# Kernel tuning notes

Hardware: AMD Instinct MI355X
Metric: run time of the kernel (lower is better)

The kernel has to match this reference:

```python
import jax, jax.numpy as jnp
import numpy as np

NB, NL, V, VOCAB, D, TOPK = 16, 64, 16384, 32000, 256, 16
NITER, EARLY, RW = 8, 2, 0.8


def setup_inputs():
    key = jax.random.key(0)
    ks = jax.random.split(key, 8)
    probas = jax.random.uniform(ks[0], (NB, NL, V), dtype=jnp.float32) + 1e-6
    h_d = jax.random.normal(ks[1], (NB, NL, D), dtype=jnp.float32)
    lengths = jax.random.randint(ks[2], (NB,), NL // 2, NL + 1)
    mask = (jnp.arange(NL)[None, :] < lengths[:, None]).astype(jnp.int32)  # prefix mask
    batch_vocab = jax.random.randint(ks[3], (V,), 0, VOCAB)
    emb_table = jax.random.normal(ks[4], (VOCAB, D), dtype=jnp.float32) * 0.02
    W1 = jax.random.normal(ks[5], (2 * D, D), dtype=jnp.float32) * 0.006
    b1 = jnp.zeros((D,), dtype=jnp.float32)
    return {"probas": probas, "h_d": h_d, "mask": mask, "batch_vocab": batch_vocab,
            "emb_table": emb_table, "W1": W1, "b1": b1}


def _forward(probas, h_d, mask, batch_vocab, emb_table, W1, b1):
    maskf = mask.astype(probas.dtype)
    MAP = jnp.argmax(probas, axis=-1)                       # [nb,nl]
    topk_vals, topk_idx = jax.lax.top_k(probas, TOPK)       # [nb,nl,K]
    topk_vals = jnp.where(mask[..., None] < 1, 1.0, topk_vals)
    logits = jnp.log(topk_vals)                             # Categorical(probs) == categorical(log p)
    sLens = jnp.sum(mask, axis=1)                           # [nb]
    one_hot = jnp.arange(NL)[None, :] == (sLens - 1)[:, None]  # one_hot_by_mask: last valid pos
    m2d = (mask[:, :, None] * mask[:, None, :]) > 0
    eyeM = jnp.eye(NL, dtype=probas.dtype)
    h_masked = h_d * maskf[..., None]

    def step(carry, k):
        max_score, best, count, stopped = carry
        choice = jax.random.categorical(k, logits)          # [nb,nl]
        samples = jnp.take_along_axis(topk_idx, choice[..., None], axis=-1)[..., 0]
        samples = jnp.where(one_hot, MAP, samples)
        embs = emb_table[batch_vocab[samples]] * maskf[..., None]   # gather+embed, masked
        new_embs = jax.nn.relu(jnp.concatenate([embs, h_masked], axis=-1) @ W1 + b1)
        Kmat = jnp.einsum('bld,bmd->blm', new_embs, new_embs)       # [nb,nl,nl]
        # det of leading lxl submatrix == det with padded rows/cols replaced by identity
        score = jnp.linalg.det(jnp.where(m2d, Kmat, eyeM))          # [nb]
        improved = score > max_score
        any_imp = jnp.any(improved)
        count = jnp.where(any_imp, 0, count + 1)
        upd = improved & (~stopped)
        stopped = stopped | ((~any_imp) & (count >= EARLY))
        max_score = jnp.where(upd, score, max_score)
        best = jnp.where(upd[:, None], samples, best)
        return (max_score, best, count, stopped), None

    init = (jnp.full((NB,), -jnp.inf, probas.dtype), MAP, jnp.int32(0), jnp.bool_(False))
    keys = jax.random.split(jax.random.key(42), NITER)
    (max_score, best, _, _), _ = jax.lax.scan(step, init, keys)

    # diverse_proba: scatter redist_weight at best choice, (1-rw) elsewhere, renormalize
    am = jnp.where(jnp.arange(V)[None, None, :] == best[:, :, None], RW, 1.0 - RW).astype(probas.dtype)
    x = probas * am
    nm = jnp.sum(x, axis=-1, keepdims=True)
    nm = jnp.where(maskf[..., None] == 0, 1e-10, nm)
    return x / nm, max_score


def reference(probas, h_d, mask, batch_vocab, emb_table, W1, b1):
    return _forward(probas, h_d, mask, batch_vocab, emb_table, W1, b1)
```

## Files before the change

### kernel.cpp

```cpp
#include <hip/hip_runtime.h>
#include <math.h>
#include <stdint.h>


#define TINYF 1.17549435082228750797e-38f

struct Keys16 { uint32_t k[16]; };

__host__ __device__ inline void tf2x32(uint32_t k0, uint32_t k1,
                                       uint32_t x0, uint32_t x1,
                                       uint32_t* o0, uint32_t* o1) {
  uint32_t ks2 = k0 ^ k1 ^ 0x1BD11BDAu;
  uint32_t ks[3] = {k0, k1, ks2};
  uint32_t v0 = x0 + k0, v1 = x1 + k1;
  const int R0[4] = {13, 15, 26, 6};
  const int R1[4] = {17, 29, 16, 24};
#pragma unroll
  for (int g = 0; g < 5; ++g) {
    const int* RR = (g & 1) ? R1 : R0;
#pragma unroll
    for (int r = 0; r < 4; ++r) {
      v0 += v1;
      v1 = (v1 << RR[r]) | (v1 >> (32 - RR[r]));
      v1 ^= v0;
    }
    v0 += ks[(g + 1) % 3];
    v1 += ks[(g + 2) % 3] + (uint32_t)(g + 1);
  }
  *o0 = v0; *o1 = v1;
}

__device__ inline float logf_ref(float x) { return (float)log((double)x); }

__device__ inline void wsync() {
  asm volatile("s_waitcnt lgkmcnt(0)" ::: "memory");
  __builtin_amdgcn_sched_barrier(0);
}

__device__ inline unsigned long long u64max(unsigned long long a,
                                            unsigned long long b) {
  return (a > b) ? a : b;
}

__global__ __launch_bounds__(256) void k_topk(const float* __restrict__ probas,
                                              const int* __restrict__ mask,
                                              int* __restrict__ topk_idx,
                                              float* __restrict__ logits,
                                              float* __restrict__ S) {
  int row = blockIdx.x;
  int t = threadIdx.x;
  const float* p = probas + (size_t)row * 16384;
  __shared__ unsigned long long lists[256][16];
  __shared__ float swsum[4];
  __shared__ int lcnt;
  unsigned long long* cand = &lists[0][0];

  cand[t] = 0ull;
  cand[t + 256] = 0ull;
  if (t == 0) lcnt = 0;
  __syncthreads();

  const uint32_t TB = 0x3F7E0000u;
  float sum = 0.f;
  const float4* p4 = (const float4*)p;
#pragma unroll 4
  for (int j = 0; j < 16; ++j) {
    float4 x = p4[t + j * 256];
    int v0 = (t + j * 256) * 4;
    uint32_t u0 = __float_as_uint(x.x), u1 = __float_as_uint(x.y);
    uint32_t u2 = __float_as_uint(x.z), u3 = __float_as_uint(x.w);
    sum += x.x; sum += x.y; sum += x.z; sum += x.w;
    uint32_t um = max(max(u0, u1), max(u2, u3));
    if (um >= TB) {
      if (u0 >= TB) { int s = atomicAdd(&lcnt, 1); if (s < 512)
          cand[s] = ((unsigned long long)u0 << 32) | (unsigned)(~(v0 + 0)); }
      if (u1 >= TB) { int s = atomicAdd(&lcnt, 1); if (s < 512)
          cand[s] = ((unsigned long long)u1 << 32) | (unsigned)(~(v0 + 1)); }
      if (u2 >= TB) { int s = atomicAdd(&lcnt, 1); if (s < 512)
          cand[s] = ((unsigned long long)u2 << 32) | (unsigned)(~(v0 + 2)); }
      if (u3 >= TB) { int s = atomicAdd(&lcnt, 1); if (s < 512)
          cand[s] = ((unsigned long long)u3 << 32) | (unsigned)(~(v0 + 3)); }
    }
  }
#pragma unroll
  for (int off = 32; off >= 1; off >>= 1) sum += __shfl_down(sum, off);
  if ((t & 63) == 0) swsum[t >> 6] = sum;
  __syncthreads();
  if (t == 0) S[row] = ((swsum[0] + swsum[1]) + swsum[2]) + swsum[3];

  int n = lcnt;
  if (n >= 16 && n <= 512) {
    if (t < 64) {
      unsigned long long c[8];
#pragma unroll
      for (int k = 0; k < 8; ++k) c[k] = cand[t + 64 * k];
      unsigned long long win = 0ull;
#pragma unroll
      for (int r = 0; r < 16; ++r) {
        unsigned long long m = c[0];
#pragma unroll
        for (int k = 1; k < 8; ++k) m = u64max(m, c[k]);
#pragma unroll
        for (int off = 32; off >= 1; off >>= 1) {
          unsigned long long o = __shfl_xor(m, off);
          m = u64max(m, o);
        }
        if (t == r) win = m;
#pragma unroll
        for (int k = 0; k < 8; ++k) if (c[k] == m) c[k] = 0ull;
      }
      if (t < 16) {
        int idx = (int)(~(unsigned)(win & 0xFFFFFFFFull));
        float val = __uint_as_float((unsigned)(win >> 32));
        topk_idx[row * 16 + t] = idx;
        logits[row * 16 + t] = (mask[row] == 0) ? 0.0f : logf_ref(val);
      }
    }
    return;
  }

  {
    unsigned long long loc[16];
#pragma unroll
    for (int q = 0; q < 16; ++q) loc[q] = 0ull;
    for (int j = 0; j < 64; ++j) {
      int v = t + j * 256;
      float x = p[v];
      unsigned long long key =
          ((unsigned long long)__float_as_uint(x) << 32) | (unsigned)(~v);
      if (key > loc[15]) {
        loc[15] = key;
#pragma unroll
        for (int q = 15; q > 0; --q) {
          if (loc[q] > loc[q - 1]) {
            unsigned long long tmp = loc[q]; loc[q] = loc[q - 1]; loc[q - 1] = tmp;
          }
        }
      }
    }
    __syncthreads();
#pragma unroll
    for (int q = 0; q < 16; ++q) lists[t][q] = loc[q];
    __syncthreads();
    for (int nl = 128; nl >= 1; nl >>= 1) {
      if (t < nl) {
        unsigned long long M[16];
        int ia = 0, ib = 0;
#pragma unroll
        for (int q = 0; q < 16; ++q) {
          unsigned long long av = lists[t][ia];
          unsigned long long bv = lists[t + nl][ib];
          if (av >= bv) { M[q] = av; ia++; } else { M[q] = bv; ib++; }
        }
#pragma unroll
        for (int q = 0; q < 16; ++q) lists[t][q] = M[q];
      }
      __syncthreads();
    }
    if (t < 16) {
      unsigned long long key = lists[0][t];
      int idx = (int)(~(unsigned)(key & 0xFFFFFFFFull));
      float val = __uint_as_float((unsigned)(key >> 32));
      topk_idx[row * 16 + t] = idx;
      logits[row * 16 + t] = (mask[row] == 0) ? 0.0f : logf_ref(val);
    }
  }
}

__global__ __launch_bounds__(256) void k_sample(Keys16 keys,
                                                const int* __restrict__ mask,
                                                const int* __restrict__ topk_idx,
                                                const float* __restrict__ logits,
                                                int* __restrict__ samples,
                                                int* __restrict__ choice) {
  int tid = blockIdx.x * 256 + threadIdx.x;
  int i = tid >> 10;
  int rbl = tid & 1023;
  int b = rbl >> 6;
  int l = rbl & 63;
  uint32_t k0 = keys.k[2 * i], k1 = keys.k[2 * i + 1];
  int sl = 0;
  for (int m = 0; m < 64; ++m) sl += mask[b * 64 + m];
  float bestv = 0.f; int bestk = 0;
#pragma unroll
  for (int k = 0; k < 16; ++k) {
    uint32_t j = (uint32_t)((b * 64 + l) * 16 + k);
    uint32_t y0, y1;
    tf2x32(k0, k1, 0u, j, &y0, &y1);
    uint32_t bits = y0 ^ y1;
    float f = __uint_as_float((bits >> 9) | 0x3f800000u) - 1.0f;
    float u = fmaxf(TINYF, f * 1.0f + TINYF);
    float t1 = logf_ref(u);
    float g = -logf_ref(-t1);
    float sv = g + logits[rbl * 16 + k];
    if (k == 0 || sv > bestv) { bestv = sv; bestk = k; }
  }
  int ce = (l == sl - 1) ? 0 : bestk;
  choice[tid] = ce;
  samples[tid] = topk_idx[rbl * 16 + ce];
}

__global__ __launch_bounds__(256) void k_ce(const int* __restrict__ topk_idx,
                                            const int* __restrict__ batch_vocab,
                                            const float* __restrict__ emb,
                                            const float* __restrict__ W1,
                                            const float* __restrict__ h_d,
                                            const float* __restrict__ b1,
                                            const int* __restrict__ mask,
                                            float* __restrict__ Eall) {
  int row = blockIdx.x;
  int t = threadIdx.x;
  __shared__ int rid[16];
  __shared__ float e[16][256];
  __shared__ float hl[256];
  float mkf = (float)mask[row];
  if (t < 16) rid[t] = batch_vocab[topk_idx[row * 16 + t]];
  hl[t] = h_d[(size_t)row * 256 + t] * mkf;
  __syncthreads();
#pragma unroll
  for (int k = 0; k < 16; ++k) e[k][t] = emb[(size_t)rid[k] * 256 + t];
  __syncthreads();
  float acch = 0.f;
  for (int j0 = 0; j0 < 256; j0 += 4) {
    float4 hv = *(const float4*)&hl[j0];
    float w0 = W1[(256 + j0 + 0) * 256 + t];
    float w1 = W1[(256 + j0 + 1) * 256 + t];
    float w2 = W1[(256 + j0 + 2) * 256 + t];
    float w3 = W1[(256 + j0 + 3) * 256 + t];
    acch = fmaf(hv.x, w0, acch);
    acch = fmaf(hv.y, w1, acch);
    acch = fmaf(hv.z, w2, acch);
    acch = fmaf(hv.w, w3, acch);
  }
  float acc[16];
#pragma unroll
  for (int k = 0; k < 16; ++k) acc[k] = 0.f;
  for (int j0 = 0; j0 < 256; j0 += 4) {
    float w0 = W1[(j0 + 0) * 256 + t];
    float w1 = W1[(j0 + 1) * 256 + t];
    float w2 = W1[(j0 + 2) * 256 + t];
    float w3 = W1[(j0 + 3) * 256 + t];
#pragma unroll
    for (int k = 0; k < 16; ++k) {
      float4 ev = *(const float4*)&e[k][j0];
      acc[k] = fmaf(ev.x, w0, acc[k]);
      acc[k] = fmaf(ev.y, w1, acc[k]);
      acc[k] = fmaf(ev.z, w2, acc[k]);
      acc[k] = fmaf(ev.w, w3, acc[k]);
    }
  }
  float b1v = b1[t];
#pragma unroll
  for (int k = 0; k < 16; ++k) {
    float val = fmaf(mkf, acc[k], acch) + b1v;
    Eall[((size_t)row * 16 + k) * 256 + t] = fmaxf(val, 0.0f);
  }
}

__global__ __launch_bounds__(256) void k_gram(const float* __restrict__ Eall,
                                              const int* __restrict__ mask,
                                              const int* __restrict__ choice,
                                              float* __restrict__ scores) {
  int blk = blockIdx.x;
  int i = blk >> 4, b = blk & 15;
  int t = threadIdx.x;
  __shared__ __align__(16) float Ett[64][68];
  __shared__ __align__(16) float Km[64][68];
  __shared__ int ch[64];
  int mskv = 0;
  if (t < 64) {
    ch[t] = choice[i * 1024 + b * 64 + t];
    mskv = mask[b * 64 + t];
  }
  __syncthreads();
  int l = t & 63, wd = t >> 6;
  const float* eptr =
      Eall + ((size_t)((b * 64 + l) * 16 + ch[l])) * 256 + wd * 16;
  float acc[16];
#pragma unroll
  for (int q = 0; q < 16; ++q) acc[q] = 0.f;
  int tx = t & 15, ty = t >> 4;
  for (int dt = 0; dt < 4; ++dt) {
    const float* src = eptr + dt * 64;
    float4 v0 = *(const float4*)(src + 0);
    float4 v1 = *(const float4*)(src + 4);
    float4 v2 = *(const float4*)(src + 8);
    float4 v3 = *(const float4*)(src + 12);
    int d0 = wd * 16;
    Ett[d0 +  0][l] = v0.x; Ett[d0 +  1][l] = v0.y;
    Ett[d0 +  2][l] = v0.z; Ett[d0 +  3][l] = v0.w;
    Ett[d0 +  4][l] = v1.x; Ett[d0 +  5][l] = v1.y;
    Ett[d0 +  6][l] = v1.z; Ett[d0 +  7][l] = v1.w;
    Ett[d0 +  8][l] = v2.x; Ett[d0 +  9][l] = v2.y;
    Ett[d0 + 10][l] = v2.z; Ett[d0 + 11][l] = v2.w;
    Ett[d0 + 12][l] = v3.x; Ett[d0 + 13][l] = v3.y;
    Ett[d0 + 14][l] = v3.z; Ett[d0 + 15][l] = v3.w;
    __syncthreads();
#pragma unroll 4
    for (int dd = 0; dd < 64; ++dd) {
      float4 av4 = *(const float4*)&Ett[dd][tx * 4];
      float4 bv4 = *(const float4*)&Ett[dd][ty * 4];
      float avv[4] = {av4.x, av4.y, av4.z, av4.w};
      float bvv[4] = {bv4.x, bv4.y, bv4.z, bv4.w};
#pragma unroll
      for (int a2 = 0; a2 < 4; ++a2)
#pragma unroll
        for (int c2 = 0; c2 < 4; ++c2)
          acc[a2 * 4 + c2] = fmaf(avv[a2], bvv[c2], acc[a2 * 4 + c2]);
    }
    __syncthreads();
  }
#pragma unroll
  for (int a2 = 0; a2 < 4; ++a2)
#pragma unroll
    for (int c2 = 0; c2 < 4; ++c2)
      Km[tx * 4 + a2][ty * 4 + c2] = acc[a2 * 4 + c2];
  __syncthreads();
  if (t >= 64) return;

  unsigned long long bal = __ballot(mskv != 0);
  int L = __popcll(bal);
  float sdet = 1.f, ssign = 1.f;
  for (int p = 0; p < L; ++p) {
    float avp = fabsf(Km[t][p]);
    unsigned long long key = 0ull;
    if (t >= p && t < L)
      key = ((unsigned long long)__float_as_uint(avp) << 32) | (unsigned)(~t);
#pragma unroll
    for (int off = 32; off >= 1; off >>= 1) {
      unsigned long long o = __shfl_xor(key, off);
      if (o > key) key = o;
    }
    int rb = (int)(~(unsigned)(key & 0xFFFFFFFFull)) & 63;
    if (rb != p) {
      ssign = -ssign;
      float x = Km[p][t];
      float y = Km[rb][t];
      Km[p][t] = y;
      Km[rb][t] = x;
    }
    wsync();
    float kpp = Km[p][p];
    sdet *= kpp;
    if (t > p && t < L) {
      float f = (kpp != 0.f) ? (Km[t][p] / kpp) : 0.f;
      float nf = -f;
      int c0 = (p + 1) & ~3;
      for (int c = c0; c < L; c += 4) {
        float4 pr = *(const float4*)&Km[p][c];
        float4 tr = *(float4*)&Km[t][c];
        tr.x = fmaf(nf, pr.x, tr.x);
        tr.y = fmaf(nf, pr.y, tr.y);
        tr.z = fmaf(nf, pr.z, tr.z);
        tr.w = fmaf(nf, pr.w, tr.w);
        *(float4*)&Km[t][c] = tr;
      }
    }
    wsync();
  }
  if (t == 0) scores[i * 16 + b] = sdet * ssign;
}

__global__ void k_select(const float* __restrict__ scores,
                         int* __restrict__ win,
                         float* __restrict__ out_ms) {
  if (threadIdx.x == 0 && blockIdx.x == 0) {
    float ms[16]; int w[16];
    for (int b = 0; b < 16; ++b) { ms[b] = -INFINITY; w[b] = -1; }
    int count = 0; bool stopped = false;
    for (int i = 0; i < 8; ++i) {
      bool any = false; bool imp[16];
      for (int b = 0; b < 16; ++b) {
        imp[b] = scores[i * 16 + b] > ms[b];
        any = any || imp[b];
      }
      count = any ? 0 : (count + 1);
      for (int b = 0; b < 16; ++b) {
        if (imp[b] && !stopped) { ms[b] = scores[i * 16 + b]; w[b] = i; }
      }
      stopped = stopped || ((!any) && (count >= 2));
    }
    for (int b = 0; b < 16; ++b) { win[b] = w[b]; out_ms[b] = ms[b]; }
  }
}

__global__ __launch_bounds__(256) void k_out(const float* __restrict__ probas,
                                             const int* __restrict__ mask,
                                             const int* __restrict__ samples,
                                             const int* __restrict__ topk_idx,
                                             const int* __restrict__ win,
                                             const float* __restrict__ S,
                                             float* __restrict__ out) {
  int row = blockIdx.x;
  int b = row >> 6;
  int t = threadIdx.x;
  int wi = win[b];
  int best = (wi >= 0) ? samples[wi * 1024 + row] : topk_idx[row * 16];
  const float* p = probas + (size_t)row * 16384;
  float* o = out + (size_t)row * 16384;
  float nm;
  if (mask[row] == 0) {
    nm = 1e-10f;
  } else {
    nm = 0.2f * S[row] + 0.6f * p[best];
  }
  const float4* p4 = (const float4*)p;
  float4* o4 = (float4*)o;
  for (int f = t; f < 4096; f += 256) {
    float4 x = p4[f];
    int v0 = f << 2;
    float4 r;
    r.x = x.x * ((v0 + 0 == best) ? 0.8f : 0.2f) / nm;
    r.y = x.y * ((v0 + 1 == best) ? 0.8f : 0.2f) / nm;
    r.z = x.z * ((v0 + 2 == best) ? 0.8f : 0.2f) / nm;
    r.w = x.w * ((v0 + 3 == best) ? 0.8f : 0.2f) / nm;
    o4[f] = r;
  }
}

extern "C" void kernel_launch(void* const* d_in, const int* in_sizes, int n_in,
                              void* d_out, int out_size, void* d_ws, size_t ws_size,
                              hipStream_t stream) {
  const float* probas = (const float*)d_in[0];
  const float* h_d    = (const float*)d_in[1];
  const int*   mask   = (const int*)d_in[2];
  const int*   bvoc   = (const int*)d_in[3];
  const float* emb    = (const float*)d_in[4];
  const float* W1     = (const float*)d_in[5];
  const float* b1     = (const float*)d_in[6];
  float* out = (float*)d_out;

  char* w = (char*)d_ws;
  int*   topk_idx = (int*)w;   w += 16384 * sizeof(int);
  float* logits   = (float*)w; w += 16384 * sizeof(float);
  float* S        = (float*)w; w += 1024 * sizeof(float);
  int*   samples  = (int*)w;   w += 8192 * sizeof(int);
  int*   choice   = (int*)w;   w += 8192 * sizeof(int);
  float* scores   = (float*)w; w += 128 * sizeof(float);
  int*   win      = (int*)w;   w += 16 * sizeof(int);

  float* Eall = out;

  Keys16 keys;
  for (uint32_t i = 0; i < 8; ++i) {
    uint32_t a, bq;
    tf2x32(0u, 42u, 0u, i, &a, &bq);
    keys.k[2 * i] = a; keys.k[2 * i + 1] = bq;
  }

  k_topk<<<1024, 256, 0, stream>>>(probas, mask, topk_idx, logits, S);
  k_sample<<<32, 256, 0, stream>>>(keys, mask, topk_idx, logits, samples, choice);
  k_ce<<<1024, 256, 0, stream>>>(topk_idx, bvoc, emb, W1, h_d, b1, mask, Eall);
  k_gram<<<128, 256, 0, stream>>>(Eall, mask, choice, scores);
  k_select<<<1, 64, 0, stream>>>(scores, win, out + 16777216);
  k_out<<<1024, 256, 0, stream>>>(probas, mask, samples, topk_idx, win, S, out);
}
```

Before: 327.8 us.

## Use implicit row pivoting with register column and swizzled LDS in determinant

The LU determinant no longer swaps rows in shared memory. Each lane tracks its logical pivot position, keeps its current pivot-column value in a register, and gets the pivot via a shuffle. This drops one sync per step, the swap traffic and the column reads. The Km array also uses an XOR-swizzled layout to reduce LDS bank conflicts on row-wise float4 accesses, at the cost of more index arithmetic and a different pivot tie-break key.

```diff
diff --git a/kernel.cpp b/kernel.cpp
--- a/kernel.cpp
+++ b/kernel.cpp
@@ -4,6 +4,8 @@
 
 
 #define TINYF 1.17549435082228750797e-38f
+
+#define KMX(r, c) (((r) * 68) + ((c) ^ ((((r) >> 3) & 7) << 2)))
 
 struct Keys16 { uint32_t k[16]; };
 
@@ -265,7 +267,7 @@
   int i = blk >> 4, b = blk & 15;
   int t = threadIdx.x;
   __shared__ __align__(16) float Ett[64][68];
-  __shared__ __align__(16) float Km[64][68];
+  __shared__ __align__(16) float KmF[64 * 68];
   __shared__ int ch[64];
   int mskv = 0;
   if (t < 64) {
@@ -314,46 +316,55 @@
   for (int a2 = 0; a2 < 4; ++a2)
 #pragma unroll
     for (int c2 = 0; c2 < 4; ++c2)
-      Km[tx * 4 + a2][ty * 4 + c2] = acc[a2 * 4 + c2];
+      KmF[KMX(tx * 4 + a2, ty * 4 + c2)] = acc[a2 * 4 + c2];
   __syncthreads();
   if (t >= 64) return;
 
   unsigned long long bal = __ballot(mskv != 0);
   int L = __popcll(bal);
+
   float sdet = 1.f, ssign = 1.f;
+  int pos = t;
+  float curcol = KmF[KMX(t, 0)];
+
   for (int p = 0; p < L; ++p) {
-    float avp = fabsf(Km[t][p]);
-    unsigned long long key = 0ull;
-    if (t >= p && t < L)
-      key = ((unsigned long long)__float_as_uint(avp) << 32) | (unsigned)(~t);
+    bool cnd = (pos >= p) && (pos < L);
+    unsigned lo = (((unsigned)(63 - pos)) << 6) | (unsigned)t;
+    unsigned long long key =
+        cnd ? ((((unsigned long long)__float_as_uint(fabsf(curcol))) << 32) | lo)
+            : 0ull;
 #pragma unroll
     for (int off = 32; off >= 1; off >>= 1) {
       unsigned long long o = __shfl_xor(key, off);
       if (o > key) key = o;
     }
-    int rb = (int)(~(unsigned)(key & 0xFFFFFFFFull)) & 63;
-    if (rb != p) {
-      ssign = -ssign;
-      float x = Km[p][t];
-      float y = Km[rb][t];
-      Km[p][t] = y;
-      Km[rb][t] = x;
-    }
-    wsync();
-    float kpp = Km[p][p];
+    int lane_rb = (int)(key & 63u);
+    int pb = 63 - (int)((key >> 6) & 63u);
+    float kpp = __shfl(curcol, lane_rb);
     sdet *= kpp;
-    if (t > p && t < L) {
-      float f = (kpp != 0.f) ? (Km[t][p] / kpp) : 0.f;
+    if (pb != p) ssign = -ssign;
+    int np = pos;
+    if (pos == p) np = pb;
+    if (t == lane_rb) np = p;
+    pos = np;
+    bool active = (pos > p) && (pos < L);
+    if (active) {
+      float f = (kpp != 0.f) ? (curcol / kpp) : 0.f;
       float nf = -f;
       int c0 = (p + 1) & ~3;
+      int sel = (p + 1) & 3;
       for (int c = c0; c < L; c += 4) {
-        float4 pr = *(const float4*)&Km[p][c];
-        float4 tr = *(float4*)&Km[t][c];
+        float4 pr = *(const float4*)&KmF[KMX(lane_rb, c)];
+        float4 tr = *(float4*)&KmF[KMX(t, c)];
         tr.x = fmaf(nf, pr.x, tr.x);
         tr.y = fmaf(nf, pr.y, tr.y);
         tr.z = fmaf(nf, pr.z, tr.z);
         tr.w = fmaf(nf, pr.w, tr.w);
-        *(float4*)&Km[t][c] = tr;
+        *(float4*)&KmF[KMX(t, c)] = tr;
+        if (c == c0) {
+          curcol = (sel == 0) ? tr.x : (sel == 1) ? tr.y
+                 : (sel == 2) ? tr.z : tr.w;
+        }
       }
     }
     wsync();
```

Result: faster. 314.5 us (-4.1%).
